# Performance work log

Hardware: AMD Instinct MI355X
Metric: run time of the kernel (lower is better)

## Reference

```python
import jax, jax.numpy as jnp
import numpy as np
from jax import lax

WS = 8      # window size (square)
SS = 4      # shift size
HEADS = 8
K = 9       # snake-conv kernel size
CENTER = K // 2
EXT = 1.0   # extend_scope


def _shift_attn_mask(H, W):
    # static numpy construction of Swin shift mask -> [num_windows, L, L]
    m = np.zeros((H, W), dtype=np.float32)
    cnt = 0
    for hs in [(0, -WS), (-WS, -SS), (-SS, None)]:
        for ws_ in [(0, -WS), (-WS, -SS), (-SS, None)]:
            m[hs[0]:hs[1], ws_[0]:ws_[1]] = cnt
            cnt += 1
    m = m.reshape(H // WS, WS, W // WS, WS).transpose(0, 2, 1, 3).reshape(-1, WS * WS)
    d = m[:, None, :] - m[:, :, None]
    return jnp.asarray(np.where(d != 0, -100.0, 0.0).astype(np.float32))


def shifted_window_attention(x, qkv_w, qkv_b, proj_w, proj_b, rel_bias):
    B, H, W, C = x.shape
    d = C // HEADS
    x = jnp.roll(x, shift=(-SS, -SS), axis=(1, 2))
    nH, nW = H // WS, W // WS
    nwin, L = nH * nW, WS * WS
    # window partition -> [B*nwin, L, C]
    xw = x.reshape(B, nH, WS, nW, WS, C).transpose(0, 1, 3, 2, 4, 5).reshape(B * nwin, L, C)
    qkv = (xw @ qkv_w.T + qkv_b).reshape(B * nwin, L, 3, HEADS, d).transpose(2, 0, 3, 1, 4)
    q, k, v = qkv[0] * (d ** -0.5), qkv[1], qkv[2]
    attn = jnp.einsum('nhld,nhmd->nhlm', q, k) + rel_bias[None]
    amask = _shift_attn_mask(H, W)  # [nwin, L, L]
    attn = attn.reshape(B, nwin, HEADS, L, L) + amask[None, :, None]
    attn = jax.nn.softmax(attn.reshape(B * nwin, HEADS, L, L), axis=-1)
    out = jnp.einsum('nhlm,nhmd->nhld', attn, v).transpose(0, 2, 1, 3).reshape(B * nwin, L, C)
    out = out @ proj_w.T + proj_b
    out = out.reshape(B, nH, nW, WS, WS, C).transpose(0, 1, 3, 2, 4, 5).reshape(B, H, W, C)
    return jnp.roll(out, shift=(SS, SS), axis=(1, 2))


def snake_coordinate_map(offset):
    # offset [B, 2K, Wd, Hd], morph=0: cumulative y offsets from the kernel center
    B, _, Wd, Hd = offset.shape
    y_off = offset[:, :K]
    # y_new[center]=0; y_new[center+i]=sum_{j=1..i} y_off[center+j]; mirror below
    up = jnp.cumsum(y_off[:, CENTER + 1:], axis=1)
    down = jnp.cumsum(y_off[:, :CENTER][:, ::-1], axis=1)[:, ::-1]
    y_cum = jnp.concatenate([down, jnp.zeros((B, 1, Wd, Hd), offset.dtype), up], axis=1)
    y_center = jnp.arange(Wd, dtype=offset.dtype)[None, None, :, None]
    y_new = y_center + EXT * y_cum                              # [B,K,Wd,Hd]
    x_spread = jnp.linspace(-CENTER, CENTER, K, dtype=offset.dtype)[None, :, None, None]
    x_center = jnp.arange(Hd, dtype=offset.dtype)[None, None, None, :]
    x_new = jnp.broadcast_to(x_center + x_spread, (B, K, Wd, Hd))
    # rearrange 'b k w h -> b (w k) h'
    y_map = y_new.transpose(0, 2, 1, 3).reshape(B, Wd * K, Hd)
    x_map = x_new.transpose(0, 2, 1, 3).reshape(B, Wd * K, Hd)
    return y_map, x_map


def bilinear_sample(feat, ymap, xmap):
    Hin, Win = feat.shape[-2], feat.shape[-1]
    y = jnp.clip(ymap, 0.0, Hin - 1.0)
    x = jnp.clip(xmap, 0.0, Win - 1.0)
    y0f, x0f = jnp.floor(y), jnp.floor(x)
    wy, wx = y - y0f, x - x0f
    y0 = y0f.astype(jnp.int32); x0 = x0f.astype(jnp.int32)
    y1 = jnp.minimum(y0 + 1, Hin - 1); x1 = jnp.minimum(x0 + 1, Win - 1)
    g = jax.vmap(lambda f, yy, xx: f[:, yy, xx])  # -> [B,C,Ho,Wo]
    v00 = g(feat, y0, x0); v01 = g(feat, y0, x1)
    v10 = g(feat, y1, x0); v11 = g(feat, y1, x1)
    wy = wy[:, None]; wx = wx[:, None]
    return v00 * (1 - wy) * (1 - wx) + v01 * (1 - wy) * wx + v10 * wy * (1 - wx) + v11 * wy * wx


def _forward(x, qkv_weight, qkv_bias, proj_weight, proj_bias, rel_bias, offset, dsc_weight, dsc_bias):
    y = shifted_window_attention(x, qkv_weight, qkv_bias, proj_weight, proj_bias, rel_bias)
    feat = y.transpose(0, 3, 1, 2)                      # NCHW
    ymap, xmap = snake_coordinate_map(offset)
    samp = bilinear_sample(feat, ymap, xmap)            # [B,C,H*K,W]
    out = lax.conv_general_dilated(samp, dsc_weight, window_strides=(K, 1), padding='VALID',
                                   dimension_numbers=('NCHW', 'OIHW', 'NCHW'))
    return jax.nn.relu(out + dsc_bias[None, :, None, None])


def setup_inputs() -> dict:
    key = jax.random.key(0)
    ks = jax.random.split(key, 9)
    B, H, W, C = 8, 64, 64, 256
    return {
        'x': jax.random.normal(ks[0], (B, H, W, C), jnp.float32),
        'qkv_weight': jax.random.normal(ks[1], (3 * C, C), jnp.float32) * 0.05,
        'qkv_bias': jax.random.normal(ks[2], (3 * C,), jnp.float32) * 0.05,
        'proj_weight': jax.random.normal(ks[3], (C, C), jnp.float32) * 0.05,
        'proj_bias': jax.random.normal(ks[4], (C,), jnp.float32) * 0.05,
        'rel_bias': jax.random.normal(ks[5], (HEADS, WS * WS, WS * WS), jnp.float32) * 0.05,
        'offset': jax.random.normal(ks[6], (B, 2 * K, H, W), jnp.float32),
        'dsc_weight': jax.random.normal(ks[7], (C, C, K, 1), jnp.float32) * 0.02,
        'dsc_bias': jax.random.normal(ks[8], (C,), jnp.float32) * 0.02,
    }


def reference(x, qkv_weight, qkv_bias, proj_weight, proj_bias, rel_bias, offset, dsc_weight, dsc_bias):
    return _forward(x, qkv_weight, qkv_bias, proj_weight, proj_bias, rel_bias, offset, dsc_weight, dsc_bias)
```

## Files before the change

kernel.cpp:

```cpp
#include <hip/hip_runtime.h>
#include <math.h>


#define NFLOAT_BUF 8388608

typedef float f32x4 __attribute__((ext_vector_type(4)));
typedef __bf16 bf16x8 __attribute__((ext_vector_type(8)));
typedef _Float16 f16x8 __attribute__((ext_vector_type(8)));

__device__ inline unsigned pack2_bf16(float a, float b) {
    union { float f; unsigned u; } ua, ub;
    ua.f = a; ub.f = b;
    unsigned ra = (ua.u + 0x7FFFu + ((ua.u >> 16) & 1u)) >> 16;
    unsigned rb = (ub.u + 0x7FFFu + ((ub.u >> 16) & 1u)) & 0xFFFF0000u;
    return (ra & 0xFFFFu) | rb;
}
__device__ inline unsigned short pack1_bf16(float a) {
    union { float f; unsigned u; } v;
    v.f = a;
    return (unsigned short)((v.u + 0x7FFFu + ((v.u >> 16) & 1u)) >> 16);
}

__global__ __launch_bounds__(256) void cvt_bf16_kernel(const float* __restrict__ src,
                                                       unsigned short* __restrict__ dst,
                                                       int n8) {
    int t = blockIdx.x * 256 + threadIdx.x;
    if (t >= n8) return;
    const float4* s = (const float4*)(src + (size_t)t * 8);
    float4 a = s[0], b = s[1];
    uint4 o;
    o.x = pack2_bf16(a.x, a.y); o.y = pack2_bf16(a.z, a.w);
    o.z = pack2_bf16(b.x, b.y); o.w = pack2_bf16(b.z, b.w);
    *(uint4*)(dst + (size_t)t * 8) = o;
}

__global__ __launch_bounds__(256) void transpose_w_kernel(const float* __restrict__ w,
                                                          unsigned short* __restrict__ wT) {
    int t = blockIdx.x * 256 + threadIdx.x;
    int o = t / 2304;
    int kk = t - o * 2304;
    int k = kk >> 8, i = kk & 255;
    wT[t] = pack1_bf16(w[(o * 256 + i) * 9 + k]);
}

__global__ __launch_bounds__(256) void ymap_kernel(const float* __restrict__ offset,
                                                   float* __restrict__ ymap) {
    int t = blockIdx.x * 256 + threadIdx.x;
    int hd = t & 63;
    int wd = (t >> 6) & 63;
    int b  = t >> 12;
    const float* op = offset + ((size_t)(b * 18) * 64 + wd) * 64 + hd;
    float yo[9];
    #pragma unroll
    for (int k = 0; k < 9; ++k) yo[k] = op[(size_t)k * 4096];
    float cum[9];
    cum[4] = 0.0f;
    float s = 0.0f;
    for (int j = 3; j >= 0; --j) { s += yo[j]; cum[j] = s; }
    s = 0.0f;
    for (int j = 5; j < 9; ++j) { s += yo[j]; cum[j] = s; }
    float wdf = (float)wd;
    float* yp = ymap + ((size_t)(b * 576 + wd * 9)) * 64 + hd;
    #pragma unroll
    for (int k = 0; k < 9; ++k) yp[(size_t)k * 64] = wdf + cum[k];
}

__global__ __launch_bounds__(256) void qkv_mfma_kernel(
    const unsigned short* __restrict__ xb, const unsigned short* __restrict__ wb,
    const float* __restrict__ qkv_b,
    _Float16* __restrict__ qh, _Float16* __restrict__ kh, _Float16* __restrict__ vt) {

    __shared__ __align__(16) char Asb[8192];
    __shared__ __align__(16) char Bsb[32768];
    __shared__ unsigned rowoff[64];

    int nb = blockIdx.x;
    int m0 = blockIdx.y * 64;
    int tid = threadIdx.x;
    int lane = tid & 63, w = tid >> 6;
    int gw = m0 >> 6;

    if (tid < 64) {
        int l = tid;
        int b = gw >> 6, win = gw & 63;
        int rh = ((win >> 3) << 3) + (l >> 3);
        int rw = ((win & 7) << 3) + (l & 7);
        int sh = (rh + 4) & 63, sw = (rw + 4) & 63;
        rowoff[l] = (unsigned)(((b * 64 + sh) * 64 + sw) * 512);
    }

    f32x4 acc[4][4];
    #pragma unroll
    for (int m = 0; m < 4; ++m)
        #pragma unroll
        for (int n = 0; n < 4; ++n) {
            f32x4 z = {0.0f, 0.0f, 0.0f, 0.0f};
            acc[m][n] = z;
        }

    const char* xc = (const char*)xb;
    const char* wc = (const char*)wb;
    int rA = (lane & 15) * 128;
    int u0 = (((lane >> 4)    ) ^ (lane & 7)) << 4;
    int u1 = ((4 + (lane >> 4)) ^ (lane & 7)) << 4;

    __syncthreads();

    for (int c = 0; c < 4; ++c) {
        #pragma unroll
        for (int r = 0; r < 2; ++r) {
            int pos = r * 256 + tid;
            int row = pos >> 3, u = pos & 7;
            const char* src = xc + rowoff[row] + c * 128 + ((u ^ (row & 7)) << 4);
            __builtin_amdgcn_global_load_lds(
                (const __attribute__((address_space(1))) unsigned int*)src,
                (__attribute__((address_space(3))) unsigned int*)(Asb + pos * 16),
                16, 0, 0);
        }
        #pragma unroll
        for (int r = 0; r < 8; ++r) {
            int pos = r * 256 + tid;
            int n = pos >> 3, u = pos & 7;
            const char* src = wc + (size_t)(nb * 256 + n) * 512 + c * 128 + ((u ^ (n & 7)) << 4);
            __builtin_amdgcn_global_load_lds(
                (const __attribute__((address_space(1))) unsigned int*)src,
                (__attribute__((address_space(3))) unsigned int*)(Bsb + pos * 16),
                16, 0, 0);
        }
        __syncthreads();

        bf16x8 av[4][2], bv[4][2];
        #pragma unroll
        for (int m = 0; m < 4; ++m) {
            av[m][0] = *(const bf16x8*)(Asb + m * 2048 + rA + u0);
            av[m][1] = *(const bf16x8*)(Asb + m * 2048 + rA + u1);
        }
        #pragma unroll
        for (int n = 0; n < 4; ++n) {
            bv[n][0] = *(const bf16x8*)(Bsb + w * 8192 + n * 2048 + rA + u0);
            bv[n][1] = *(const bf16x8*)(Bsb + w * 8192 + n * 2048 + rA + u1);
        }
        #pragma unroll
        for (int m = 0; m < 4; ++m)
            #pragma unroll
            for (int n = 0; n < 4; ++n) {
                acc[m][n] = __builtin_amdgcn_mfma_f32_16x16x32_bf16(av[m][0], bv[n][0], acc[m][n], 0, 0, 0);
                acc[m][n] = __builtin_amdgcn_mfma_f32_16x16x32_bf16(av[m][1], bv[n][1], acc[m][n], 0, 0, 0);
            }
        __syncthreads();
    }

    float scale = (nb == 0) ? 0.17677669529663689f : 1.0f;
    #pragma unroll
    for (int nf = 0; nf < 4; ++nf) {
        int o = w * 64 + nf * 16 + (lane & 15);
        float bias = qkv_b[nb * 256 + o];
        int hh = o >> 5, dd = o & 31;
        if (nb < 2) {
            _Float16* dstb = (nb == 0) ? qh : kh;
            _Float16* base = dstb + ((size_t)(gw * 8 + hh) * 64) * 32 + dd;
            #pragma unroll
            for (int mf = 0; mf < 4; ++mf) {
                int l0 = mf * 16 + (lane >> 4) * 4;
                #pragma unroll
                for (int j = 0; j < 4; ++j)
                    base[(size_t)(l0 + j) * 32] = (_Float16)((acc[mf][nf][j] + bias) * scale);
            }
        } else {
            _Float16* base = vt + ((size_t)(gw * 8 + hh) * 32 + dd) * 64;
            #pragma unroll
            for (int mf = 0; mf < 4; ++mf) {
                int l0 = mf * 16 + (lane >> 4) * 4;
                union { _Float16 x[4]; uint2 u; } pk;
                #pragma unroll
                for (int j = 0; j < 4; ++j) pk.x[j] = (_Float16)(acc[mf][nf][j] + bias);
                *(uint2*)(base + l0) = pk.u;
            }
        }
    }
}

__global__ __launch_bounds__(512) void attn_mfma_kernel(
    const _Float16* __restrict__ qh, const _Float16* __restrict__ kh,
    const _Float16* __restrict__ vt, const float* __restrict__ rel_bias,
    unsigned short* __restrict__ attn_ob) {

    __shared__ __align__(16) char Plds[65536];
    int n = blockIdx.x;
    int win = n & 63;
    int wy = win >> 3, wx = win & 7;
    int tid = threadIdx.x, lane = tid & 63, h = tid >> 6;
    int qc = lane & 15, g = lane >> 4;
    char* P = Plds + h * 8192;

    const _Float16* qp = qh + (size_t)(n * 8 + h) * 2048;
    const _Float16* kp = kh + (size_t)(n * 8 + h) * 2048;
    const _Float16* vp = vt + (size_t)(n * 8 + h) * 2048;
    const float* rb = rel_bias + (size_t)h * 4096;

    int rk[16];
    #pragma unroll
    for (int mt = 0; mt < 4; ++mt)
        #pragma unroll
        for (int j = 0; j < 4; ++j) {
            int key = mt * 16 + g * 4 + j;
            int rh = wy * 8 + (key >> 3), rw = wx * 8 + (key & 7);
            rk[mt * 4 + j] = (rh < 56 ? 0 : (rh < 60 ? 1 : 2)) * 3
                           + (rw < 56 ? 0 : (rw < 60 ? 1 : 2));
        }

    f16x8 kf[4];
    #pragma unroll
    for (int mt = 0; mt < 4; ++mt)
        kf[mt] = *(const f16x8*)(kp + (mt * 16 + qc) * 32 + g * 8);

    #pragma unroll
    for (int nt = 0; nt < 4; ++nt) {
        int q = nt * 16 + qc;
        int rqh = wy * 8 + (q >> 3), rqw = wx * 8 + (q & 7);
        int rq = (rqh < 56 ? 0 : (rqh < 60 ? 1 : 2)) * 3
               + (rqw < 56 ? 0 : (rqw < 60 ? 1 : 2));
        f16x8 qf = *(const f16x8*)(qp + q * 32 + g * 8);

        f32x4 s[4];
        #pragma unroll
        for (int mt = 0; mt < 4; ++mt) {
            f32x4 z = {0.0f, 0.0f, 0.0f, 0.0f};
            s[mt] = __builtin_amdgcn_mfma_f32_16x16x32_f16(kf[mt], qf, z, 0, 0, 0);
        }

        float vals[16];
        #pragma unroll
        for (int mt = 0; mt < 4; ++mt) {
            float4 bv4 = *(const float4*)(rb + q * 64 + mt * 16 + g * 4);
            vals[mt * 4 + 0] = s[mt][0] + bv4.x + (rk[mt * 4 + 0] != rq ? -100.0f : 0.0f);
            vals[mt * 4 + 1] = s[mt][1] + bv4.y + (rk[mt * 4 + 1] != rq ? -100.0f : 0.0f);
            vals[mt * 4 + 2] = s[mt][2] + bv4.z + (rk[mt * 4 + 2] != rq ? -100.0f : 0.0f);
            vals[mt * 4 + 3] = s[mt][3] + bv4.w + (rk[mt * 4 + 3] != rq ? -100.0f : 0.0f);
        }

        float mx = vals[0];
        #pragma unroll
        for (int i = 1; i < 16; ++i) mx = fmaxf(mx, vals[i]);
        mx = fmaxf(mx, __shfl_xor(mx, 16));
        mx = fmaxf(mx, __shfl_xor(mx, 32));

        float sum = 0.0f;
        #pragma unroll
        for (int i = 0; i < 16; ++i) { vals[i] = __expf(vals[i] - mx); sum += vals[i]; }
        sum += __shfl_xor(sum, 16);
        sum += __shfl_xor(sum, 32);
        float inv = 1.0f / sum;

        #pragma unroll
        for (int mt = 0; mt < 4; ++mt) {
            union { _Float16 x[4]; uint2 u; } pk4;
            #pragma unroll
            for (int j = 0; j < 4; ++j) pk4.x[j] = (_Float16)(vals[mt * 4 + j] * inv);
            int off = (mt * 32 + g * 8) ^ ((q & 7) << 4);
            *(uint2*)(P + q * 128 + off) = pk4.u;
        }
    }

    f16x8 pa[4][2];
    #pragma unroll
    for (int im = 0; im < 4; ++im)
        #pragma unroll
        for (int ks = 0; ks < 2; ++ks) {
            int row = im * 16 + qc;
            int off = (ks * 64 + g * 16) ^ ((row & 7) << 4);
            pa[im][ks] = *(const f16x8*)(P + row * 128 + off);
        }
    f16x8 bvv[2][2];
    #pragma unroll
    for (int in = 0; in < 2; ++in)
        #pragma unroll
        for (int ks = 0; ks < 2; ++ks)
            bvv[in][ks] = *(const f16x8*)(vp + (in * 16 + qc) * 64 + ks * 32 + g * 8);

    f32x4 acc[4][2];
    #pragma unroll
    for (int im = 0; im < 4; ++im)
        #pragma unroll
        for (int in = 0; in < 2; ++in) {
            f32x4 z = {0.0f, 0.0f, 0.0f, 0.0f};
            acc[im][in] = z;
        }
    #pragma unroll
    for (int im = 0; im < 4; ++im)
        #pragma unroll
        for (int in = 0; in < 2; ++in) {
            acc[im][in] = __builtin_amdgcn_mfma_f32_16x16x32_f16(pa[im][0], bvv[in][0], acc[im][in], 0, 0, 0);
            acc[im][in] = __builtin_amdgcn_mfma_f32_16x16x32_f16(pa[im][1], bvv[in][1], acc[im][in], 0, 0, 0);
        }

    #pragma unroll
    for (int im = 0; im < 4; ++im)
        #pragma unroll
        for (int in = 0; in < 2; ++in)
            #pragma unroll
            for (int j = 0; j < 4; ++j) {
                int q2 = im * 16 + g * 4 + j;
                attn_ob[(size_t)(n * 64 + q2) * 256 + h * 32 + in * 16 + qc] =
                    pack1_bf16(acc[im][in][j]);
            }
}

__global__ __launch_bounds__(256) void proj_mfma_kernel(
    const unsigned short* __restrict__ attn_ob, const unsigned short* __restrict__ pwb,
    const float* __restrict__ proj_b, unsigned short* __restrict__ featb) {

    __shared__ __align__(16) char Asb[8192];
    __shared__ __align__(16) char Bsb[32768];

    int m0 = blockIdx.x * 64;
    int tid = threadIdx.x;
    int lane = tid & 63, w = tid >> 6;
    int gw = m0 >> 6;
    int bidx = gw >> 6, win = gw & 63;

    f32x4 acc[4][4];
    #pragma unroll
    for (int m = 0; m < 4; ++m)
        #pragma unroll
        for (int n = 0; n < 4; ++n) {
            f32x4 z = {0.0f, 0.0f, 0.0f, 0.0f};
            acc[m][n] = z;
        }

    const char* ac = (const char*)attn_ob;
    const char* wc = (const char*)pwb;
    int rA = (lane & 15) * 128;
    int u0 = (((lane >> 4)    ) ^ (lane & 7)) << 4;
    int u1 = ((4 + (lane >> 4)) ^ (lane & 7)) << 4;

    for (int c = 0; c < 4; ++c) {
        #pragma unroll
        for (int r = 0; r < 2; ++r) {
            int pos = r * 256 + tid;
            int row = pos >> 3, u = pos & 7;
            const char* src = ac + (size_t)(m0 + row) * 512 + c * 128 + ((u ^ (row & 7)) << 4);
            __builtin_amdgcn_global_load_lds(
                (const __attribute__((address_space(1))) unsigned int*)src,
                (__attribute__((address_space(3))) unsigned int*)(Asb + pos * 16),
                16, 0, 0);
        }
        #pragma unroll
        for (int r = 0; r < 8; ++r) {
            int pos = r * 256 + tid;
            int n = pos >> 3, u = pos & 7;
            const char* src = wc + (size_t)n * 512 + c * 128 + ((u ^ (n & 7)) << 4);
            __builtin_amdgcn_global_load_lds(
                (const __attribute__((address_space(1))) unsigned int*)src,
                (__attribute__((address_space(3))) unsigned int*)(Bsb + pos * 16),
                16, 0, 0);
        }
        __syncthreads();

        bf16x8 av[4][2], bv[4][2];
        #pragma unroll
        for (int m = 0; m < 4; ++m) {
            av[m][0] = *(const bf16x8*)(Asb + m * 2048 + rA + u0);
            av[m][1] = *(const bf16x8*)(Asb + m * 2048 + rA + u1);
        }
        #pragma unroll
        for (int n = 0; n < 4; ++n) {
            bv[n][0] = *(const bf16x8*)(Bsb + w * 8192 + n * 2048 + rA + u0);
            bv[n][1] = *(const bf16x8*)(Bsb + w * 8192 + n * 2048 + rA + u1);
        }
        #pragma unroll
        for (int m = 0; m < 4; ++m)
            #pragma unroll
            for (int n = 0; n < 4; ++n) {
                acc[m][n] = __builtin_amdgcn_mfma_f32_16x16x32_bf16(av[m][0], bv[n][0], acc[m][n], 0, 0, 0);
                acc[m][n] = __builtin_amdgcn_mfma_f32_16x16x32_bf16(av[m][1], bv[n][1], acc[m][n], 0, 0, 0);
            }
        __syncthreads();
    }

    #pragma unroll
    for (int nf = 0; nf < 4; ++nf) {
        int f = w * 64 + nf * 16 + (lane & 15);
        float bias = proj_b[f];
        #pragma unroll
        for (int mf = 0; mf < 4; ++mf) {
            #pragma unroll
            for (int j = 0; j < 4; ++j) {
                int px = mf * 16 + (lane >> 4) * 4 + j;
                int rh = ((win >> 3) << 3) + (px >> 3);
                int rw = ((win & 7) << 3) + (px & 7);
                int p = (rh + 4) & 63;
                int qq = (rw + 4) & 63;
                featb[((size_t)(bidx * 64 + p) * 64 + qq) * 256 + f] =
                    pack1_bf16(acc[mf][nf][j] + bias);
            }
        }
    }
}

__global__ __launch_bounds__(256) void sample_conv_mfma_kernel(
    const unsigned short* __restrict__ featb, const float* __restrict__ ymap,
    const unsigned short* __restrict__ wT2, const float* __restrict__ dsc_b,
    float* __restrict__ out) {

    __shared__ __align__(16) char Asb[8192];
    __shared__ __align__(16) char Bsb[32768];
    __shared__ unsigned row0[9][64];
    __shared__ unsigned row1[9][64];
    __shared__ float    wyv[9][64];

    int blk = blockIdx.x;
    int b = blk >> 6, wd = blk & 63;
    int tid = threadIdx.x;
    int lane = tid & 63, w = tid >> 6;

    for (int idx = tid; idx < 576; idx += 256) {
        int k = idx >> 6, hd = idx & 63;
        float y = ymap[((size_t)(b * 576 + wd * 9 + k)) * 64 + hd];
        y = fminf(fmaxf(y, 0.0f), 63.0f);
        float y0f = floorf(y);
        int y0 = (int)y0f;
        int y1 = min(y0 + 1, 63);
        int xc = min(max(hd + k - 4, 0), 63);
        row0[k][hd] = (unsigned)(((b * 64 + y0) * 64 + xc) * 512);
        row1[k][hd] = (unsigned)(((b * 64 + y1) * 64 + xc) * 512);
        wyv[k][hd] = y - y0f;
    }

    f32x4 acc[4][4];
    #pragma unroll
    for (int m = 0; m < 4; ++m)
        #pragma unroll
        for (int n = 0; n < 4; ++n) {
            f32x4 z = {0.0f, 0.0f, 0.0f, 0.0f};
            acc[m][n] = z;
        }

    const char* featc = (const char*)featb;
    const char* wc    = (const char*)wT2;

    int pxA0 = tid >> 3;
    int sA   = tid & 7;
    int rA = (lane & 15) * 128;
    int u0 = (((lane >> 4)    ) ^ (lane & 7)) << 4;
    int u1 = ((4 + (lane >> 4)) ^ (lane & 7)) << 4;

    __syncthreads();

    for (int c = 0; c < 36; ++c) {
        #pragma unroll
        for (int r = 0; r < 8; ++r) {
            int pos = r * 256 + tid;
            int n = pos >> 3, uu = pos & 7;
            int s = uu ^ (n & 7);
            const char* src = wc + n * 4608 + c * 128 + s * 16;
            __builtin_amdgcn_global_load_lds(
                (const __attribute__((address_space(1))) unsigned int*)src,
                (__attribute__((address_space(3))) unsigned int*)(Bsb + pos * 16),
                16, 0, 0);
        }
        int ks  = c >> 2;
        int cib = (c & 3) * 128;
        #pragma unroll
        for (int r = 0; r < 2; ++r) {
            int px = pxA0 + r * 32;
            unsigned b0 = row0[ks][px] + cib + sA * 16;
            unsigned b1 = row1[ks][px] + cib + sA * 16;
            float wy = wyv[ks][px];
            float om = 1.0f - wy;
            uint4 v0 = *(const uint4*)(featc + b0);
            uint4 v1 = *(const uint4*)(featc + b1);
            const unsigned* q0 = (const unsigned*)&v0;
            const unsigned* q1 = (const unsigned*)&v1;
            uint4 o4;
            unsigned* qo = (unsigned*)&o4;
            #pragma unroll
            for (int j = 0; j < 4; ++j) {
                union { unsigned u; float f; } alo, ahi, blo, bhi;
                alo.u = q0[j] << 16; ahi.u = q0[j] & 0xFFFF0000u;
                blo.u = q1[j] << 16; bhi.u = q1[j] & 0xFFFF0000u;
                float rlo = alo.f * om + blo.f * wy;
                float rhi = ahi.f * om + bhi.f * wy;
                qo[j] = pack2_bf16(rlo, rhi);
            }
            *(uint4*)(Asb + px * 128 + ((sA ^ (px & 7)) << 4)) = o4;
        }
        __syncthreads();

        bf16x8 av[4][2], bv[4][2];
        #pragma unroll
        for (int m = 0; m < 4; ++m) {
            av[m][0] = *(const bf16x8*)(Asb + m * 2048 + rA + u0);
            av[m][1] = *(const bf16x8*)(Asb + m * 2048 + rA + u1);
        }
        #pragma unroll
        for (int n = 0; n < 4; ++n) {
            bv[n][0] = *(const bf16x8*)(Bsb + w * 8192 + n * 2048 + rA + u0);
            bv[n][1] = *(const bf16x8*)(Bsb + w * 8192 + n * 2048 + rA + u1);
        }
        #pragma unroll
        for (int m = 0; m < 4; ++m)
            #pragma unroll
            for (int n = 0; n < 4; ++n) {
                acc[m][n] = __builtin_amdgcn_mfma_f32_16x16x32_bf16(av[m][0], bv[n][0], acc[m][n], 0, 0, 0);
                acc[m][n] = __builtin_amdgcn_mfma_f32_16x16x32_bf16(av[m][1], bv[n][1], acc[m][n], 0, 0, 0);
            }
        __syncthreads();
    }

    #pragma unroll
    for (int n = 0; n < 4; ++n) {
        int o = w * 64 + n * 16 + (lane & 15);
        float bvs = dsc_b[o];
        float* orow = out + ((size_t)(b * 256 + o) * 64 + wd) * 64;
        #pragma unroll
        for (int m = 0; m < 4; ++m) {
            int px = m * 16 + (lane >> 4) * 4;
            float4 res;
            res.x = fmaxf(acc[m][n][0] + bvs, 0.0f);
            res.y = fmaxf(acc[m][n][1] + bvs, 0.0f);
            res.z = fmaxf(acc[m][n][2] + bvs, 0.0f);
            res.w = fmaxf(acc[m][n][3] + bvs, 0.0f);
            *(float4*)(orow + px) = res;
        }
    }
}

extern "C" void kernel_launch(void* const* d_in, const int* in_sizes, int n_in,
                              void* d_out, int out_size, void* d_ws, size_t ws_size,
                              hipStream_t stream) {
    (void)in_sizes; (void)n_in; (void)out_size; (void)ws_size;
    const float* x        = (const float*)d_in[0];
    const float* qkv_w    = (const float*)d_in[1];
    const float* qkv_b    = (const float*)d_in[2];
    const float* proj_w   = (const float*)d_in[3];
    const float* proj_b   = (const float*)d_in[4];
    const float* rel_bias = (const float*)d_in[5];
    const float* offset   = (const float*)d_in[6];
    const float* dsc_w    = (const float*)d_in[7];
    const float* dsc_b    = (const float*)d_in[8];
    float* out = (float*)d_out;

    unsigned short* wsu = (unsigned short*)d_ws;
    _Float16* qh = (_Float16*)wsu;
    _Float16* kh = (_Float16*)(wsu + NFLOAT_BUF);
    _Float16* vt = (_Float16*)(wsu + 2 * (size_t)NFLOAT_BUF);
    unsigned short* attn_ob = wsu + 3 * (size_t)NFLOAT_BUF;
    unsigned short* featb   = wsu + 4 * (size_t)NFLOAT_BUF;
    unsigned short* xb      = wsu + 5 * (size_t)NFLOAT_BUF;
    unsigned short* wb      = wsu + 6 * (size_t)NFLOAT_BUF;
    unsigned short* pwb     = wb + 196608;
    unsigned short* wT2     = pwb + 65536;
    float* ymap = (float*)(wT2 + 589824);

    cvt_bf16_kernel<<<4096, 256, 0, stream>>>(x, xb, 1048576);
    cvt_bf16_kernel<<<96, 256, 0, stream>>>(qkv_w, wb, 24576);
    cvt_bf16_kernel<<<32, 256, 0, stream>>>(proj_w, pwb, 8192);
    transpose_w_kernel<<<2304, 256, 0, stream>>>(dsc_w, wT2);
    ymap_kernel<<<128, 256, 0, stream>>>(offset, ymap);
    qkv_mfma_kernel<<<dim3(3, 512), 256, 0, stream>>>(xb, wb, qkv_b, qh, kh, vt);
    attn_mfma_kernel<<<512, 512, 0, stream>>>(qh, kh, vt, rel_bias, attn_ob);
    proj_mfma_kernel<<<512, 256, 0, stream>>>(attn_ob, pwb, proj_b, featb);
    sample_conv_mfma_kernel<<<512, 256, 0, stream>>>(featb, ymap, wT2, dsc_b, out);
}
```

Baseline: 225.2 us.

## Double-buffer snake-conv gather, switch to fp16 math, load weights directly to registers

The sampled-conv kernel now double-buffers the interpolated activation tile in LDS, so the gather for chunk c+1 overlaps the MFMA work on chunk c. Weights are read straight from global memory into registers instead of being staged in LDS. Features and conv weights are stored in fp16, so the bilinear blend runs as packed half-precision vector math with no bf16 unpacking. The block index mapping is also swapped so that neighbouring blocks cover different batches at the same row. Risks are lower blend precision in fp16, possible fp16 overflow of feature values, and less coalesced, uncached-in-LDS weight reads repeated per wave.

```diff
diff --git a/kernel.cpp b/kernel.cpp
--- a/kernel.cpp
+++ b/kernel.cpp
@@ -35,12 +35,12 @@
 }
 
 __global__ __launch_bounds__(256) void transpose_w_kernel(const float* __restrict__ w,
-                                                          unsigned short* __restrict__ wT) {
+                                                          _Float16* __restrict__ wT) {
     int t = blockIdx.x * 256 + threadIdx.x;
     int o = t / 2304;
     int kk = t - o * 2304;
     int k = kk >> 8, i = kk & 255;
-    wT[t] = pack1_bf16(w[(o * 256 + i) * 9 + k]);
+    wT[t] = (_Float16)w[(o * 256 + i) * 9 + k];
 }
 
 __global__ __launch_bounds__(256) void ymap_kernel(const float* __restrict__ offset,
@@ -308,7 +308,7 @@
 
 __global__ __launch_bounds__(256) void proj_mfma_kernel(
     const unsigned short* __restrict__ attn_ob, const unsigned short* __restrict__ pwb,
-    const float* __restrict__ proj_b, unsigned short* __restrict__ featb) {
+    const float* __restrict__ proj_b, _Float16* __restrict__ feath) {
 
     __shared__ __align__(16) char Asb[8192];
     __shared__ __align__(16) char Bsb[32768];
@@ -391,28 +391,28 @@
                 int rw = ((win & 7) << 3) + (px & 7);
                 int p = (rh + 4) & 63;
                 int qq = (rw + 4) & 63;
-                featb[((size_t)(bidx * 64 + p) * 64 + qq) * 256 + f] =
-                    pack1_bf16(acc[mf][nf][j] + bias);
-            }
-        }
-    }
-}
-
-__global__ __launch_bounds__(256) void sample_conv_mfma_kernel(
-    const unsigned short* __restrict__ featb, const float* __restrict__ ymap,
-    const unsigned short* __restrict__ wT2, const float* __restrict__ dsc_b,
+                feath[((size_t)(bidx * 64 + p) * 64 + qq) * 256 + f] =
+                    (_Float16)(acc[mf][nf][j] + bias);
+            }
+        }
+    }
+}
+
+__global__ __launch_bounds__(256) void sample_conv_mfma2_kernel(
+    const _Float16* __restrict__ feath, const float* __restrict__ ymap,
+    const _Float16* __restrict__ wT2h, const float* __restrict__ dsc_b,
     float* __restrict__ out) {
 
-    __shared__ __align__(16) char Asb[8192];
-    __shared__ __align__(16) char Bsb[32768];
+    __shared__ __align__(16) char Asb[2][8192];
     __shared__ unsigned row0[9][64];
     __shared__ unsigned row1[9][64];
     __shared__ float    wyv[9][64];
 
     int blk = blockIdx.x;
-    int b = blk >> 6, wd = blk & 63;
+    int b = blk & 7, wd = blk >> 3;
     int tid = threadIdx.x;
     int lane = tid & 63, w = tid >> 6;
+    int qc = lane & 15, g = lane >> 4;
 
     for (int idx = tid; idx < 576; idx += 256) {
         int k = idx >> 6, hd = idx & 63;
@@ -436,86 +436,107 @@
             acc[m][n] = z;
         }
 
-    const char* featc = (const char*)featb;
-    const char* wc    = (const char*)wT2;
+    const char* featc = (const char*)feath;
+    const char* wc    = (const char*)wT2h;
 
     int pxA0 = tid >> 3;
     int sA   = tid & 7;
-    int rA = (lane & 15) * 128;
-    int u0 = (((lane >> 4)    ) ^ (lane & 7)) << 4;
-    int u1 = ((4 + (lane >> 4)) ^ (lane & 7)) << 4;
+    int rA = qc * 128;
+    int u0 = ((g    ) ^ (lane & 7)) << 4;
+    int u1 = ((4 + g) ^ (lane & 7)) << 4;
+
+    const char* wrow[4];
+    #pragma unroll
+    for (int n = 0; n < 4; ++n)
+        wrow[n] = wc + (size_t)(w * 64 + n * 16 + qc) * 4608 + g * 16;
+
+    f16x8 s0[2], s1[2];
+    float swy[2];
 
     __syncthreads();
 
-    for (int c = 0; c < 36; ++c) {
-        #pragma unroll
-        for (int r = 0; r < 8; ++r) {
-            int pos = r * 256 + tid;
-            int n = pos >> 3, uu = pos & 7;
-            int s = uu ^ (n & 7);
-            const char* src = wc + n * 4608 + c * 128 + s * 16;
-            __builtin_amdgcn_global_load_lds(
-                (const __attribute__((address_space(1))) unsigned int*)src,
-                (__attribute__((address_space(3))) unsigned int*)(Bsb + pos * 16),
-                16, 0, 0);
-        }
-        int ks  = c >> 2;
-        int cib = (c & 3) * 128;
+    {
+        int ks = 0, cib = 0;
         #pragma unroll
         for (int r = 0; r < 2; ++r) {
             int px = pxA0 + r * 32;
             unsigned b0 = row0[ks][px] + cib + sA * 16;
             unsigned b1 = row1[ks][px] + cib + sA * 16;
-            float wy = wyv[ks][px];
-            float om = 1.0f - wy;
-            uint4 v0 = *(const uint4*)(featc + b0);
-            uint4 v1 = *(const uint4*)(featc + b1);
-            const unsigned* q0 = (const unsigned*)&v0;
-            const unsigned* q1 = (const unsigned*)&v1;
-            uint4 o4;
-            unsigned* qo = (unsigned*)&o4;
-            #pragma unroll
-            for (int j = 0; j < 4; ++j) {
-                union { unsigned u; float f; } alo, ahi, blo, bhi;
-                alo.u = q0[j] << 16; ahi.u = q0[j] & 0xFFFF0000u;
-                blo.u = q1[j] << 16; bhi.u = q1[j] & 0xFFFF0000u;
-                float rlo = alo.f * om + blo.f * wy;
-                float rhi = ahi.f * om + bhi.f * wy;
-                qo[j] = pack2_bf16(rlo, rhi);
-            }
-            *(uint4*)(Asb + px * 128 + ((sA ^ (px & 7)) << 4)) = o4;
+            swy[r] = wyv[ks][px];
+            s0[r] = *(const f16x8*)(featc + b0);
+            s1[r] = *(const f16x8*)(featc + b1);
+        }
+        #pragma unroll
+        for (int r = 0; r < 2; ++r) {
+            int px = pxA0 + r * 32;
+            _Float16 wyh = (_Float16)swy[r];
+            _Float16 omh = (_Float16)(1.0f - swy[r]);
+            f16x8 res = s0[r] * omh + s1[r] * wyh;
+            *(f16x8*)(Asb[0] + px * 128 + ((sA ^ (px & 7)) << 4)) = res;
+        }
+    }
+    __syncthreads();
+
+    for (int c = 0; c < 36; ++c) {
+        int cur = c & 1;
+
+        f16x8 bv[4][2];
+        #pragma unroll
+        for (int n = 0; n < 4; ++n) {
+            bv[n][0] = *(const f16x8*)(wrow[n] + c * 128);
+            bv[n][1] = *(const f16x8*)(wrow[n] + c * 128 + 64);
+        }
+
+        if (c < 35) {
+            int cn = c + 1;
+            int ks = cn >> 2, cib = (cn & 3) * 128;
+            #pragma unroll
+            for (int r = 0; r < 2; ++r) {
+                int px = pxA0 + r * 32;
+                unsigned b0 = row0[ks][px] + cib + sA * 16;
+                unsigned b1 = row1[ks][px] + cib + sA * 16;
+                swy[r] = wyv[ks][px];
+                s0[r] = *(const f16x8*)(featc + b0);
+                s1[r] = *(const f16x8*)(featc + b1);
+            }
+        }
+
+        f16x8 av[4][2];
+        #pragma unroll
+        for (int m = 0; m < 4; ++m) {
+            av[m][0] = *(const f16x8*)(Asb[cur] + m * 2048 + rA + u0);
+            av[m][1] = *(const f16x8*)(Asb[cur] + m * 2048 + rA + u1);
+        }
+
+        #pragma unroll
+        for (int m = 0; m < 4; ++m)
+            #pragma unroll
+            for (int n = 0; n < 4; ++n) {
+                acc[m][n] = __builtin_amdgcn_mfma_f32_16x16x32_f16(av[m][0], bv[n][0], acc[m][n], 0, 0, 0);
+                acc[m][n] = __builtin_amdgcn_mfma_f32_16x16x32_f16(av[m][1], bv[n][1], acc[m][n], 0, 0, 0);
+            }
+
+        if (c < 35) {
+            #pragma unroll
+            for (int r = 0; r < 2; ++r) {
+                int px = pxA0 + r * 32;
+                _Float16 wyh = (_Float16)swy[r];
+                _Float16 omh = (_Float16)(1.0f - swy[r]);
+                f16x8 res = s0[r] * omh + s1[r] * wyh;
+                *(f16x8*)(Asb[cur ^ 1] + px * 128 + ((sA ^ (px & 7)) << 4)) = res;
+            }
         }
         __syncthreads();
-
-        bf16x8 av[4][2], bv[4][2];
-        #pragma unroll
-        for (int m = 0; m < 4; ++m) {
-            av[m][0] = *(const bf16x8*)(Asb + m * 2048 + rA + u0);
-            av[m][1] = *(const bf16x8*)(Asb + m * 2048 + rA + u1);
-        }
-        #pragma unroll
-        for (int n = 0; n < 4; ++n) {
-            bv[n][0] = *(const bf16x8*)(Bsb + w * 8192 + n * 2048 + rA + u0);
-            bv[n][1] = *(const bf16x8*)(Bsb + w * 8192 + n * 2048 + rA + u1);
-        }
-        #pragma unroll
-        for (int m = 0; m < 4; ++m)
-            #pragma unroll
-            for (int n = 0; n < 4; ++n) {
-                acc[m][n] = __builtin_amdgcn_mfma_f32_16x16x32_bf16(av[m][0], bv[n][0], acc[m][n], 0, 0, 0);
-                acc[m][n] = __builtin_amdgcn_mfma_f32_16x16x32_bf16(av[m][1], bv[n][1], acc[m][n], 0, 0, 0);
-            }
-        __syncthreads();
     }
 
     #pragma unroll
     for (int n = 0; n < 4; ++n) {
-        int o = w * 64 + n * 16 + (lane & 15);
+        int o = w * 64 + n * 16 + qc;
         float bvs = dsc_b[o];
         float* orow = out + ((size_t)(b * 256 + o) * 64 + wd) * 64;
         #pragma unroll
         for (int m = 0; m < 4; ++m) {
-            int px = m * 16 + (lane >> 4) * 4;
+            int px = m * 16 + g * 4;
             float4 res;
             res.x = fmaxf(acc[m][n][0] + bvs, 0.0f);
             res.y = fmaxf(acc[m][n][1] + bvs, 0.0f);
@@ -546,20 +567,20 @@
     _Float16* kh = (_Float16*)(wsu + NFLOAT_BUF);
     _Float16* vt = (_Float16*)(wsu + 2 * (size_t)NFLOAT_BUF);
     unsigned short* attn_ob = wsu + 3 * (size_t)NFLOAT_BUF;
-    unsigned short* featb   = wsu + 4 * (size_t)NFLOAT_BUF;
+    _Float16* feath = (_Float16*)(wsu + 4 * (size_t)NFLOAT_BUF);
     unsigned short* xb      = wsu + 5 * (size_t)NFLOAT_BUF;
     unsigned short* wb      = wsu + 6 * (size_t)NFLOAT_BUF;
     unsigned short* pwb     = wb + 196608;
-    unsigned short* wT2     = pwb + 65536;
-    float* ymap = (float*)(wT2 + 589824);
+    _Float16* wT2h          = (_Float16*)(pwb + 65536);
+    float* ymap = (float*)((unsigned short*)wT2h + 589824);
 
     cvt_bf16_kernel<<<4096, 256, 0, stream>>>(x, xb, 1048576);
     cvt_bf16_kernel<<<96, 256, 0, stream>>>(qkv_w, wb, 24576);
     cvt_bf16_kernel<<<32, 256, 0, stream>>>(proj_w, pwb, 8192);
-    transpose_w_kernel<<<2304, 256, 0, stream>>>(dsc_w, wT2);
+    transpose_w_kernel<<<2304, 256, 0, stream>>>(dsc_w, wT2h);
     ymap_kernel<<<128, 256, 0, stream>>>(offset, ymap);
     qkv_mfma_kernel<<<dim3(3, 512), 256, 0, stream>>>(xb, wb, qkv_b, qh, kh, vt);
     attn_mfma_kernel<<<512, 512, 0, stream>>>(qh, kh, vt, rel_bias, attn_ob);
-    proj_mfma_kernel<<<512, 256, 0, stream>>>(attn_ob, pwb, proj_b, featb);
-    sample_conv_mfma_kernel<<<512, 256, 0, stream>>>(featb, ymap, wT2, dsc_b, out);
-}
+    proj_mfma_kernel<<<512, 256, 0, stream>>>(attn_ob, pwb, proj_b, feath);
+    sample_conv_mfma2_kernel<<<512, 256, 0, stream>>>(feath, ymap, wT2h, dsc_b, out);
+}
```

After: 251.6 us. 1.12x slower.
